# Performance work log

Hardware: AMD Instinct MI355X
Metric: run time of the kernel (lower is better)

The kernel has to match this reference:

```python
import jax, jax.numpy as jnp
import numpy as np

N, E, D, G, F_IN, F_OUT = 100_000, 1_000_000, 64, 256, 4, 4


def _lin_init(key, fan_in, fan_out):
    k1, k2 = jax.random.split(key)
    s = 1.0 / np.sqrt(fan_in)
    W = jax.random.uniform(k1, (fan_in, fan_out), jnp.float32, -s, s)
    b = jax.random.uniform(k2, (fan_out,), jnp.float32, -s, s)
    return W, b


def setup_inputs() -> dict:
    key = jax.random.key(0)
    ks = jax.random.split(key, 10)
    x = jax.random.normal(ks[0], (N, F_IN), jnp.float32)
    edge_index = jax.random.randint(ks[1], (2, E), 0, N, jnp.int32)
    # contiguous, sorted graph ids covering all G graphs (PyG-style batch vector)
    batch_index = ((jnp.arange(N, dtype=jnp.int32) * G) // N).astype(jnp.int32)
    topo_hidden = jax.random.normal(ks[2], (N, D), jnp.float32)
    W0, b0 = _lin_init(ks[3], F_IN, D)
    W1, b1 = _lin_init(ks[4], D, D)
    W2, b2 = _lin_init(ks[5], D, D)
    W3, b3 = _lin_init(ks[6], D, D)
    Wf, bf = _lin_init(ks[7], D, D)
    Wo, bo = _lin_init(ks[8], 2 * D, F_OUT)
    return dict(x=x, edge_index=edge_index, batch_index=batch_index,
                topo_hidden=topo_hidden,
                W0=W0, b0=b0, W1=W1, b1=b1, W2=W2, b2=b2, W3=W3, b3=b3,
                Wf=Wf, bf=bf, Wo=Wo, bo=bo, num_graphs=G)


def reference(x, edge_index, batch_index, topo_hidden,
              W0, b0, W1, b1, W2, b2, W3, b3, Wf, bf, Wo, bo, num_graphs):
    n = x.shape[0]
    loops = jnp.arange(n, dtype=edge_index.dtype)
    row = jnp.concatenate([edge_index[0], loops])  # sources (+ self loops)
    col = jnp.concatenate([edge_index[1], loops])  # targets (+ self loops)
    # degree of targets, symmetric normalization (same for every layer)
    deg = jax.ops.segment_sum(jnp.ones_like(col, dtype=x.dtype), col, num_segments=n)
    dis = deg ** -0.5  # deg >= 1 thanks to self loops
    norm = dis[row] * dis[col]  # [E+N]

    def gcn(h, W, b):
        h = h @ W + b                      # dense linear
        msg = norm[:, None] * h[row]       # gather + normalize
        return jax.ops.segment_sum(msg, col, num_segments=n)  # scatter-add

    h = jnp.tanh(gcn(x, W0, b0))
    h = jnp.tanh(gcn(h, W1, b1))
    h = jnp.tanh(gcn(h, W2, b2))
    h = jnp.tanh(gcn(h, W3, b3))
    h = (topo_hidden * h) @ Wf + bf        # fusion
    gmax = jax.ops.segment_max(h, batch_index, num_segments=num_graphs)
    gsum = jax.ops.segment_sum(h, batch_index, num_segments=num_graphs)
    cnt = jax.ops.segment_sum(jnp.ones((n, 1), x.dtype), batch_index, num_segments=num_graphs)
    pooled = jnp.concatenate([gmax, gsum / cnt], axis=1)  # [G, 2D]
    out = pooled @ Wo + bo
    return out, pooled
```

## Files before the change

### kernel.cpp

```cpp
#include <hip/hip_runtime.h>
#include <hip/hip_bf16.h>

#define N_NODES 100000
#define N_EDGES 1000000
#define DIM 64
#define N_GRAPHS 256
#define F_IN 4
#define F_OUT 4
#define NBK 196
#define CAP 8192
#define BIN_CHUNK 4096

using short8 = __attribute__((ext_vector_type(8))) short;
using f32x4 = __attribute__((ext_vector_type(4))) float;

__device__ __forceinline__ float bf_lo(unsigned int u) { return __uint_as_float(u << 16); }
__device__ __forceinline__ float bf_hi(unsigned int u) { return __uint_as_float(u & 0xffff0000u); }
__device__ __forceinline__ unsigned short f2bf(float f) {
    unsigned int u = __float_as_uint(f);
    u = u + 0x7fffu + ((u >> 16) & 1u);
    return (unsigned short)(u >> 16);
}
__device__ __forceinline__ unsigned pack2(float a, float b) {
    return (unsigned)f2bf(a) | ((unsigned)f2bf(b) << 16);
}
__device__ __forceinline__ unsigned fenc(float f) {
    unsigned u = __float_as_uint(f);
    return (u >> 31) ? ~u : (u | 0x80000000u);
}

__global__ void bin_scatter(const int* __restrict__ rows, const int* __restrict__ cols,
                            int* __restrict__ bucketCursor, unsigned int* __restrict__ binned,
                            int E, int nChunks, const float* __restrict__ W1,
                            const float* __restrict__ W2, const float* __restrict__ W3,
                            const float* __restrict__ Wf, unsigned short* __restrict__ wfrag,
                            float* __restrict__ pooled) {
    __shared__ int hist[NBK];
    __shared__ int base[NBK];
    __shared__ int cnt2[NBK];
    int tid = threadIdx.x;
    if (blockIdx.x >= nChunks) {
        int widx = blockIdx.x - nChunks;
        if (widx == 4) {
            float4* p4 = (float4*)pooled;
            for (int i = tid; i < N_GRAPHS * 32; i += 256) p4[i] = make_float4(0.f, 0.f, 0.f, 0.f);
            return;
        }
        const float* W = widx == 0 ? W1 : widx == 1 ? W2 : widx == 2 ? W3 : Wf;
        for (int s = tid; s < 512; s += 256) {
            int jtkk = s >> 6, l = s & 63;
            int jt = jtkk >> 1, kk = jtkk & 1;
            int j = jt * 16 + (l & 15);
            int kbase = kk * 32 + (l >> 4) * 8;
            unsigned short* dst = wfrag + widx * 4096 + s * 8;
#pragma unroll
            for (int e = 0; e < 8; ++e) dst[e] = f2bf(W[(kbase + e) * 64 + j]);
        }
        return;
    }
    for (int i = tid; i < NBK; i += 256) { hist[i] = 0; cnt2[i] = 0; }
    __syncthreads();
    int chunk = blockIdx.x * BIN_CHUNK;
#pragma unroll
    for (int i = 0; i < 16; ++i) {
        int e = chunk + i * 256 + tid;
        if (e < E) atomicAdd(&hist[cols[e] >> 9], 1);
    }
    __syncthreads();
    for (int i = tid; i < NBK; i += 256)
        if (hist[i] > 0) base[i] = atomicAdd(&bucketCursor[i], hist[i]);
    __syncthreads();
#pragma unroll
    for (int i = 0; i < 16; ++i) {
        int e = chunk + i * 256 + tid;
        if (e < E) {
            int c = cols[e], r = rows[e];
            int b = c >> 9;
            int pos = base[b] + atomicAdd(&cnt2[b], 1);
            binned[b * CAP + pos] = ((unsigned)(c & 511) << 17) | (unsigned)r;
        }
    }
}

__global__ void bucket_fill(const unsigned int* __restrict__ binned,
                            const int* __restrict__ bucketCursor, const float* __restrict__ x,
                            int* __restrict__ csr_src, int2* __restrict__ rowse,
                            float* __restrict__ dis, uint4* __restrict__ xsp, int n) {
    __shared__ int hist[512];
    __shared__ int scn[256];
    __shared__ int cur[512];
    int b = blockIdx.x, tid = threadIdx.x;
    int nbase = b << 9;
    int ebase = b * CAP;
    hist[tid] = 0;
    hist[tid + 256] = 0;
    __syncthreads();
    int cnt = bucketCursor[b];
    for (int k = tid; k < cnt; k += 256) atomicAdd(&hist[binned[ebase + k] >> 17], 1);
    __syncthreads();
    int h0 = hist[2 * tid], h1 = hist[2 * tid + 1];
    int s = h0 + h1;
    scn[tid] = s;
    __syncthreads();
    for (int ofs = 1; ofs < 256; ofs <<= 1) {
        int u = (tid >= ofs) ? scn[tid - ofs] : 0;
        __syncthreads();
        scn[tid] += u;
        __syncthreads();
    }
    int excl = scn[tid] - s;
    int st0 = ebase + excl, st1 = ebase + excl + h0;
    cur[2 * tid] = st0;
    cur[2 * tid + 1] = st1;
    int node0 = nbase + 2 * tid, node1 = nbase + 2 * tid + 1;
    if (node0 < n) {
        rowse[node0] = make_int2(st0, st0 + h0);
        float d = rsqrtf((float)(h0 + 1));
        dis[node0] = d;
        float4 xv = ((const float4*)x)[node0];
        uint4 o;
        o.x = pack2(d * xv.x, d * xv.y);
        o.y = pack2(d * xv.z, d * xv.w);
        o.z = __float_as_uint(d);
        o.w = 0;
        xsp[node0] = o;
    }
    if (node1 < n) {
        rowse[node1] = make_int2(st1, st1 + h1);
        float d = rsqrtf((float)(h1 + 1));
        dis[node1] = d;
        float4 xv = ((const float4*)x)[node1];
        uint4 o;
        o.x = pack2(d * xv.x, d * xv.y);
        o.y = pack2(d * xv.z, d * xv.w);
        o.z = __float_as_uint(d);
        o.w = 0;
        xsp[node1] = o;
    }
    __syncthreads();
    for (int k = tid; k < cnt; k += 256) {
        unsigned v = binned[ebase + k];
        int cl = v >> 17;
        int r = (int)(v & 0x1FFFFu);
        int pos = atomicAdd(&cur[cl], 1);
        csr_src[pos] = r;
    }
}

__global__ void aggx_gemm01(const int2* __restrict__ rowse, const int* __restrict__ csr_src,
                            const uint4* __restrict__ xsp, const float* __restrict__ W0,
                            const float* __restrict__ b0, const unsigned short* __restrict__ wfrag,
                            const float* __restrict__ bias, const float* __restrict__ dis,
                            unsigned short* __restrict__ outv, int n) {
    __shared__ float W0s[256];
    __shared__ float b0s[64];
    __shared__ float4 aggL[64];
    __shared__ float nsL[64];
    int tid = threadIdx.x;
    W0s[tid] = W0[tid];
    if (tid < 64) b0s[tid] = b0[tid];
    int nodeBase = blockIdx.x * 64;
    int ln = tid >> 2, sl = tid & 3;
    int c = nodeBase + ln;
    if (c < n) {
        int2 se = rowse[c];
        float a0 = 0.f, a1 = 0.f, a2 = 0.f, a3 = 0.f, ns = 0.f;
        uint4 u0 = xsp[c];
        float dc = __uint_as_float(u0.z);
        if (sl == 0) {
            a0 = bf_lo(u0.x); a1 = bf_hi(u0.x); a2 = bf_lo(u0.y); a3 = bf_hi(u0.y);
            ns = dc;
        }
        int k = se.x + sl;
        for (; k + 4 < se.y; k += 8) {
            int r1 = csr_src[k], r2 = csr_src[k + 4];
            uint4 u1 = xsp[r1];
            uint4 u2 = xsp[r2];
            a0 += bf_lo(u1.x) + bf_lo(u2.x);
            a1 += bf_hi(u1.x) + bf_hi(u2.x);
            a2 += bf_lo(u1.y) + bf_lo(u2.y);
            a3 += bf_hi(u1.y) + bf_hi(u2.y);
            ns += __uint_as_float(u1.z) + __uint_as_float(u2.z);
        }
        if (k < se.y) {
            int r = csr_src[k];
            uint4 u = xsp[r];
            a0 += bf_lo(u.x); a1 += bf_hi(u.x); a2 += bf_lo(u.y); a3 += bf_hi(u.y);
            ns += __uint_as_float(u.z);
        }
#pragma unroll
        for (int m = 1; m < 4; m <<= 1) {
            a0 += __shfl_xor(a0, m, 64);
            a1 += __shfl_xor(a1, m, 64);
            a2 += __shfl_xor(a2, m, 64);
            a3 += __shfl_xor(a3, m, 64);
            ns += __shfl_xor(ns, m, 64);
        }
        if (sl == 0) {
            aggL[ln] = make_float4(dc * a0, dc * a1, dc * a2, dc * a3);
            nsL[ln] = dc * ns;
        }
    }
    __syncthreads();
    int wid = tid >> 6, l = tid & 63;
    int nodeBaseW = nodeBase + wid * 16;
    if (nodeBaseW >= n) return;
    int lrow = wid * 16 + (l & 15);
    float4 ax = aggL[lrow];
    float nsv = nsL[lrow];
    int kb = (l >> 4) * 8;
    short8 a0v, a1v;
#pragma unroll
    for (int e = 0; e < 8; ++e) {
        int k = kb + e;
        float g0 = nsv * b0s[k] + ax.x * W0s[k] + ax.y * W0s[64 + k] +
                   ax.z * W0s[128 + k] + ax.w * W0s[192 + k];
        a0v[e] = (short)f2bf(tanhf(g0));
        int k1 = k + 32;
        float g1 = nsv * b0s[k1] + ax.x * W0s[k1] + ax.y * W0s[64 + k1] +
                   ax.z * W0s[128 + k1] + ax.w * W0s[192 + k1];
        a1v[e] = (short)f2bf(tanhf(g1));
    }
    const short8* B = (const short8*)wfrag;
    f32x4 acc[4];
#pragma unroll
    for (int jt = 0; jt < 4; ++jt) {
        acc[jt] = (f32x4){0.f, 0.f, 0.f, 0.f};
        acc[jt] = __builtin_amdgcn_mfma_f32_16x16x32_bf16(a0v, B[(jt * 2 + 0) * 64 + l], acc[jt], 0, 0, 0);
        acc[jt] = __builtin_amdgcn_mfma_f32_16x16x32_bf16(a1v, B[(jt * 2 + 1) * 64 + l], acc[jt], 0, 0, 0);
    }
    int rbase = nodeBaseW + (l >> 4) * 4;
#pragma unroll
    for (int jt = 0; jt < 4; ++jt) {
        int j = jt * 16 + (l & 15);
        float bj = bias[j];
#pragma unroll
        for (int r = 0; r < 4; ++r) {
            int node = rbase + r;
            outv[(size_t)node * 64 + j] = f2bf((acc[jt][r] + bj) * dis[node]);
        }
    }
}

template <bool TOPO, bool POOL>
__global__ void agg_gemm(const int2* __restrict__ rowse, const int* __restrict__ csr_src,
                         const float* __restrict__ dis, const uint2* __restrict__ hs2,
                         const float* __restrict__ topo, const unsigned short* __restrict__ wfrag,
                         const float* __restrict__ bias, unsigned short* __restrict__ outv,
                         float* __restrict__ pooled) {
    __shared__ short8 actlds[128];
    int tid = threadIdx.x;
    int wid = tid >> 6, lane = tid & 63;
    int nodeBase = blockIdx.x * 16;
    int q = lane >> 4, f = lane & 15;
#pragma unroll 1
    for (int i = 0; i < 4; ++i) {
        int r = wid * 4 + i;
        int node = nodeBase + r;
        int2 se = rowse[node];
        float a0 = 0.f, a1 = 0.f, a2 = 0.f, a3 = 0.f;
        float c0 = 0.f, c1 = 0.f, c2 = 0.f, c3 = 0.f;
        if (q == 0) {
            uint2 u = hs2[(size_t)node * 16 + f];
            a0 = bf_lo(u.x); a1 = bf_hi(u.x); a2 = bf_lo(u.y); a3 = bf_hi(u.y);
        }
        int k = se.x + q;
        for (; k + 4 < se.y; k += 8) {
            int r1 = csr_src[k];
            int r2 = csr_src[k + 4];
            uint2 u1 = hs2[(size_t)r1 * 16 + f];
            uint2 u2 = hs2[(size_t)r2 * 16 + f];
            a0 += bf_lo(u1.x); a1 += bf_hi(u1.x); a2 += bf_lo(u1.y); a3 += bf_hi(u1.y);
            c0 += bf_lo(u2.x); c1 += bf_hi(u2.x); c2 += bf_lo(u2.y); c3 += bf_hi(u2.y);
        }
        if (k < se.y) {
            int rr = csr_src[k];
            uint2 u = hs2[(size_t)rr * 16 + f];
            a0 += bf_lo(u.x); a1 += bf_hi(u.x); a2 += bf_lo(u.y); a3 += bf_hi(u.y);
        }
        a0 += c0; a1 += c1; a2 += c2; a3 += c3;
#pragma unroll
        for (int m = 16; m < 64; m <<= 1) {
            a0 += __shfl_xor(a0, m, 64);
            a1 += __shfl_xor(a1, m, 64);
            a2 += __shfl_xor(a2, m, 64);
            a3 += __shfl_xor(a3, m, 64);
        }
        if (q == 0) {
            float dc = dis[node];
            float v0 = tanhf(dc * a0);
            float v1 = tanhf(dc * a1);
            float v2 = tanhf(dc * a2);
            float v3 = tanhf(dc * a3);
            if (TOPO) {
                float4 tp = ((const float4*)topo)[(size_t)node * 16 + f];
                v0 *= tp.x; v1 *= tp.y; v2 *= tp.z; v3 *= tp.w;
            }
            uint2 o;
            o.x = pack2(v0, v1);
            o.y = pack2(v2, v3);
            ((uint2*)actlds)[r * 16 + (((f >> 1) ^ (r & 7)) << 1) + (f & 1)] = o;
        }
    }
    __syncthreads();
    int rA = lane & 15, qq = lane >> 4;
    short8 av0 = actlds[rA * 8 + (qq ^ (rA & 7))];
    short8 av1 = actlds[rA * 8 + ((4 + qq) ^ (rA & 7))];
    const short8* B = (const short8*)wfrag;
    f32x4 acc = (f32x4){0.f, 0.f, 0.f, 0.f};
    acc = __builtin_amdgcn_mfma_f32_16x16x32_bf16(av0, B[(wid * 2 + 0) * 64 + lane], acc, 0, 0, 0);
    acc = __builtin_amdgcn_mfma_f32_16x16x32_bf16(av1, B[(wid * 2 + 1) * 64 + lane], acc, 0, 0, 0);
    int j = wid * 16 + rA;
    float bj = bias[j];
    int rbase = nodeBase + qq * 4;
    if (POOL) {
        float v0 = acc[0] + bj, v1 = acc[1] + bj, v2 = acc[2] + bj, v3 = acc[3] + bj;
        int glo = (int)(((long long)nodeBase << 8) / N_NODES);
        int ghi = (int)(((long long)(nodeBase + 15) << 8) / N_NODES);
        if (glo == ghi) {
            float mx = fmaxf(fmaxf(v0, v1), fmaxf(v2, v3));
            float sm = v0 + v1 + v2 + v3;
            mx = fmaxf(mx, __shfl_xor(mx, 16, 64));
            sm += __shfl_xor(sm, 16, 64);
            mx = fmaxf(mx, __shfl_xor(mx, 32, 64));
            sm += __shfl_xor(sm, 32, 64);
            if (lane < 16) {
                atomicAdd(&pooled[glo * 128 + 64 + j], sm);
                atomicMax((unsigned*)&pooled[glo * 128 + j], fenc(mx));
            }
        } else {
            float vv[4] = {v0, v1, v2, v3};
#pragma unroll
            for (int rr = 0; rr < 4; ++rr) {
                int g = (int)(((long long)(rbase + rr) << 8) / N_NODES);
                atomicAdd(&pooled[g * 128 + 64 + j], vv[rr]);
                atomicMax((unsigned*)&pooled[g * 128 + j], fenc(vv[rr]));
            }
        }
    } else {
#pragma unroll
        for (int rr = 0; rr < 4; ++rr) {
            int node = rbase + rr;
            outv[(size_t)node * 64 + j] = f2bf((acc[rr] + bj) * dis[node]);
        }
    }
}

__global__ void finalize_out(float* __restrict__ pooled, const float* __restrict__ Wo,
                             const float* __restrict__ bo, float* __restrict__ out, int n, int G) {
    __shared__ float p[128];
    int g = blockIdx.x, t = threadIdx.x;
    int start = (int)(((long long)g * n + G - 1) / G);
    int end = (int)(((long long)(g + 1) * n + G - 1) / G);
    float v;
    if (t < 64) {
        unsigned u = __float_as_uint(pooled[g * 128 + t]);
        unsigned rep = (u >> 31) ? (u & 0x7FFFFFFFu) : ~u;
        v = __uint_as_float(rep);
    } else {
        v = pooled[g * 128 + t] / (float)(end - start);
    }
    pooled[g * 128 + t] = v;
    p[t] = v;
    __syncthreads();
    if (t < F_OUT) {
        float acc = bo[t];
#pragma unroll 8
        for (int k = 0; k < 128; ++k) acc += p[k] * Wo[k * F_OUT + t];
        out[g * F_OUT + t] = acc;
    }
}

extern "C" void kernel_launch(void* const* d_in, const int* in_sizes, int n_in,
                              void* d_out, int out_size, void* d_ws, size_t ws_size,
                              hipStream_t stream) {
    const float* x = (const float*)d_in[0];
    const int* edge_index = (const int*)d_in[1];
    const float* topo = (const float*)d_in[3];
    const float* W0 = (const float*)d_in[4];
    const float* b0 = (const float*)d_in[5];
    const float* W1 = (const float*)d_in[6];
    const float* b1 = (const float*)d_in[7];
    const float* W2 = (const float*)d_in[8];
    const float* b2 = (const float*)d_in[9];
    const float* W3 = (const float*)d_in[10];
    const float* b3 = (const float*)d_in[11];
    const float* Wf = (const float*)d_in[12];
    const float* bf_ = (const float*)d_in[13];
    const float* Wo = (const float*)d_in[14];
    const float* bo = (const float*)d_in[15];

    const int* rows = edge_index;
    const int* cols = edge_index + N_EDGES;

    char* ws = (char*)d_ws;
    size_t off = 0;
    float* dis = (float*)(ws + off); off += (size_t)N_NODES * 4;
    int* bucketCursor = (int*)(ws + off); off += 1024;
    int2* rowse = (int2*)(ws + off); off += (size_t)N_NODES * 8;
    int* csr_src = (int*)(ws + off); off += (size_t)NBK * CAP * 4;
    unsigned int* binned = (unsigned int*)(ws + off); off += (size_t)NBK * CAP * 4;
    uint4* xsp = (uint4*)(ws + off); off += (size_t)N_NODES * 16;
    off = (off + 255) & ~(size_t)255;
    unsigned short* wfrag = (unsigned short*)(ws + off); off += 4 * 4096 * 2;
    off = (off + 255) & ~(size_t)255;
    unsigned short* hsA = (unsigned short*)(ws + off); off += (size_t)N_NODES * DIM * 2;
    off = (off + 255) & ~(size_t)255;
    unsigned short* hsB = (unsigned short*)(ws + off); off += (size_t)N_NODES * DIM * 2;
    (void)ws_size;

    float* out = (float*)d_out;
    float* pooled = (float*)d_out + N_GRAPHS * F_OUT;

    const int nChunks = (N_EDGES + BIN_CHUNK - 1) / BIN_CHUNK;

    hipMemsetAsync(bucketCursor, 0, NBK * 4, stream);

    bin_scatter<<<nChunks + 5, 256, 0, stream>>>(rows, cols, bucketCursor, binned, N_EDGES,
                                                 nChunks, W1, W2, W3, Wf, wfrag, pooled);
    bucket_fill<<<NBK, 256, 0, stream>>>(binned, bucketCursor, x, csr_src, rowse, dis, xsp, N_NODES);

    aggx_gemm01<<<(N_NODES + 63) / 64, 256, 0, stream>>>(
        rowse, csr_src, xsp, W0, b0, wfrag, b1, dis, hsA, N_NODES);

    const int gridF = N_NODES / 16;
    agg_gemm<false, false><<<gridF, 256, 0, stream>>>(
        rowse, csr_src, dis, (const uint2*)hsA, nullptr, wfrag + 4096, b2, hsB, nullptr);
    agg_gemm<false, false><<<gridF, 256, 0, stream>>>(
        rowse, csr_src, dis, (const uint2*)hsB, nullptr, wfrag + 2 * 4096, b3, hsA, nullptr);
    agg_gemm<true, true><<<gridF, 256, 0, stream>>>(
        rowse, csr_src, dis, (const uint2*)hsA, topo, wfrag + 3 * 4096, bf_, nullptr, pooled);

    finalize_out<<<N_GRAPHS, 128, 0, stream>>>(pooled, Wo, bo, out, N_NODES, N_GRAPHS);
}
```

Before: 206.9 us.

## Use per-wave aggregation and MFMA in middle GCN layers to avoid block syncs

Adds agg_gemm_wp, where each wave aggregates its own 4 nodes into a private LDS slice with an XOR swizzle, then runs a 16-row MFMA on that slice. This removes the block-wide barrier between aggregation and GEMM. The edge loop is also unrolled by two with separate accumulators to keep more gathers in flight. The trade-off is wasted MFMA rows (only 4 of 16 are real nodes), and only a quarter of lanes do the stores.

```diff
diff --git a/kernel.cpp b/kernel.cpp
--- a/kernel.cpp
+++ b/kernel.cpp
@@ -238,6 +238,77 @@
         for (int r = 0; r < 4; ++r) {
             int node = rbase + r;
             outv[(size_t)node * 64 + j] = f2bf((acc[jt][r] + bj) * dis[node]);
+        }
+    }
+}
+
+__global__ void agg_gemm_wp(const int2* __restrict__ rowse, const int* __restrict__ csr_src,
+                            const float* __restrict__ dis, const uint2* __restrict__ hs2,
+                            const unsigned short* __restrict__ wfrag,
+                            const float* __restrict__ bias, unsigned short* __restrict__ outv) {
+    __shared__ short8 actlds[4][32];
+    int tid = threadIdx.x;
+    int wid = tid >> 6, lane = tid & 63;
+    int nodeBase = blockIdx.x * 16 + wid * 4;
+    int q = lane >> 4, f = lane & 15;
+#pragma unroll 1
+    for (int i = 0; i < 4; ++i) {
+        int node = nodeBase + i;
+        int2 se = rowse[node];
+        float a0 = 0.f, a1 = 0.f, a2 = 0.f, a3 = 0.f;
+        float c0 = 0.f, c1 = 0.f, c2 = 0.f, c3 = 0.f;
+        if (q == 0) {
+            uint2 u = hs2[(size_t)node * 16 + f];
+            a0 = bf_lo(u.x); a1 = bf_hi(u.x); a2 = bf_lo(u.y); a3 = bf_hi(u.y);
+        }
+        int k = se.x + q;
+        for (; k + 4 < se.y; k += 8) {
+            int r1 = csr_src[k];
+            int r2 = csr_src[k + 4];
+            uint2 u1 = hs2[(size_t)r1 * 16 + f];
+            uint2 u2 = hs2[(size_t)r2 * 16 + f];
+            a0 += bf_lo(u1.x); a1 += bf_hi(u1.x); a2 += bf_lo(u1.y); a3 += bf_hi(u1.y);
+            c0 += bf_lo(u2.x); c1 += bf_hi(u2.x); c2 += bf_lo(u2.y); c3 += bf_hi(u2.y);
+        }
+        if (k < se.y) {
+            int rr = csr_src[k];
+            uint2 u = hs2[(size_t)rr * 16 + f];
+            a0 += bf_lo(u.x); a1 += bf_hi(u.x); a2 += bf_lo(u.y); a3 += bf_hi(u.y);
+        }
+        a0 += c0; a1 += c1; a2 += c2; a3 += c3;
+#pragma unroll
+        for (int m = 16; m < 64; m <<= 1) {
+            a0 += __shfl_xor(a0, m, 64);
+            a1 += __shfl_xor(a1, m, 64);
+            a2 += __shfl_xor(a2, m, 64);
+            a3 += __shfl_xor(a3, m, 64);
+        }
+        if (q == 0) {
+            float dc = dis[node];
+            uint2 o;
+            o.x = pack2(tanhf(dc * a0), tanhf(dc * a1));
+            o.y = pack2(tanhf(dc * a2), tanhf(dc * a3));
+            ((uint2*)actlds[wid])[i * 16 + (((f >> 1) ^ i) << 1) + (f & 1)] = o;
+        }
+    }
+    int rr = lane & 15, qq = lane >> 4;
+    int r3 = rr & 3;
+    short8 av0 = actlds[wid][r3 * 8 + (qq ^ r3)];
+    short8 av1 = actlds[wid][r3 * 8 + ((4 + qq) ^ r3)];
+    const short8* B = (const short8*)wfrag;
+#pragma unroll 1
+    for (int jt = 0; jt < 4; ++jt) {
+        f32x4 acc = (f32x4){0.f, 0.f, 0.f, 0.f};
+        acc = __builtin_amdgcn_mfma_f32_16x16x32_bf16(av0, B[(jt * 2 + 0) * 64 + lane], acc, 0, 0, 0);
+        acc = __builtin_amdgcn_mfma_f32_16x16x32_bf16(av1, B[(jt * 2 + 1) * 64 + lane], acc, 0, 0, 0);
+        if (qq == 0) {
+            int j = jt * 16 + rr;
+            float bj = bias[j];
+#pragma unroll
+            for (int reg = 0; reg < 4; ++reg) {
+                int node = nodeBase + reg;
+                outv[(size_t)node * 64 + j] = f2bf((acc[reg] + bj) * dis[node]);
+            }
         }
     }
 }
@@ -424,10 +495,11 @@
         rowse, csr_src, xsp, W0, b0, wfrag, b1, dis, hsA, N_NODES);
 
     const int gridF = N_NODES / 16;
-    agg_gemm<false, false><<<gridF, 256, 0, stream>>>(
-        rowse, csr_src, dis, (const uint2*)hsA, nullptr, wfrag + 4096, b2, hsB, nullptr);
-    agg_gemm<false, false><<<gridF, 256, 0, stream>>>(
-        rowse, csr_src, dis, (const uint2*)hsB, nullptr, wfrag + 2 * 4096, b3, hsA, nullptr);
+    agg_gemm_wp<<<gridF, 256, 0, stream>>>(rowse, csr_src, dis, (const uint2*)hsA,
+                                           wfrag + 4096, b2, hsB);
+    agg_gemm_wp<<<gridF, 256, 0, stream>>>(rowse, csr_src, dis, (const uint2*)hsB,
+                                           wfrag + 2 * 4096, b3, hsA);
+
     agg_gemm<true, true><<<gridF, 256, 0, stream>>>(
         rowse, csr_src, dis, (const uint2*)hsA, topo, wfrag + 3 * 4096, bf_, nullptr, pooled);
 
```

Measured after the change: 221.3 us. 1.07x slower.
